# Optimization experiments

Measured on AMD Instinct MI355X. Metric: run time of the kernel, lower is better.

Reference implementation:

```python
import jax, jax.numpy as jnp
import numpy as np

N_NODES = 100000
N_EDGES = 1200000
IN_FEATS = 30
HIDDEN = 64


def setup_inputs() -> dict:
    key = jax.random.key(0)
    k = jax.random.split(key, 6)
    x = jax.random.normal(k[0], (N_NODES, IN_FEATS), dtype=jnp.float32)
    W1 = jax.random.normal(k[1], (IN_FEATS, HIDDEN), dtype=jnp.float32) * (1.0 / np.sqrt(IN_FEATS))
    b1 = jnp.zeros((HIDDEN,), dtype=jnp.float32)
    W2 = jax.random.normal(k[2], (HIDDEN, HIDDEN), dtype=jnp.float32) * (1.0 / np.sqrt(HIDDEN))
    b2 = jnp.zeros((HIDDEN,), dtype=jnp.float32)
    src = jax.random.randint(k[3], (N_EDGES,), 0, N_NODES, dtype=jnp.int32)
    dst = jax.random.randint(k[4], (N_EDGES,), 0, N_NODES, dtype=jnp.int32)
    return {"x": x, "W1": W1, "b1": b1, "W2": W2, "b2": b2, "src": src, "dst": dst}


def _graph_conv(h, W, b, src, dst, norm_src, norm_dst, n_nodes):
    # DGL GraphConv, norm='both': D_in^{-1/2} A D_out^{-1/2} h W + b, then relu
    h = h * norm_src[:, None]          # [N, din] scale by out-degree^{-1/2}
    h = h @ W                          # [N, dout] dense transform
    agg = jax.ops.segment_sum(h[src], dst, num_segments=n_nodes)  # sparse aggregation
    return jax.nn.relu(agg * norm_dst[:, None] + b)


def reference(x, W1, b1, W2, b2, src, dst):
    n = x.shape[0]
    ones = jnp.ones(src.shape, dtype=x.dtype)
    out_deg = jax.ops.segment_sum(ones, src, num_segments=n)
    in_deg = jax.ops.segment_sum(ones, dst, num_segments=n)
    norm_src = jnp.maximum(out_deg, 1.0) ** -0.5
    norm_dst = jnp.maximum(in_deg, 1.0) ** -0.5
    h = _graph_conv(x, W1, b1, src, dst, norm_src, norm_dst, n)
    h = _graph_conv(h, W2, b2, src, dst, norm_src, norm_dst, n)
    return h
```

## Files before the change

kernel.cpp:

```cpp
#include <hip/hip_runtime.h>
#include <hip/hip_fp16.h>

constexpr int IN_FEATS = 30;
constexpr int HIDDEN   = 64;
constexpr int SCAN_CHUNK = 1024;
constexpr int RB_BITS = 9;
constexpr int RB_MASK = (1 << RB_BITS) - 1;
constexpr int ECHUNK  = 2048;
constexpr int NPB     = 32;

__global__ __launch_bounds__(256) void part_count(
    const int* __restrict__ src, const int* __restrict__ dst,
    int* __restrict__ cntT, int nE, int NBK, int NCH, int NK2)
{
    __shared__ int binsD[256], binsS[256];
    int b = blockIdx.x, t = threadIdx.x;
    binsD[t] = 0; binsS[t] = 0;
    __syncthreads();
    int base = b * ECHUNK;
#pragma unroll
    for (int i = 0; i < ECHUNK / 256; ++i) {
        int e = base + t + i * 256;
        if (e < nE) {
            atomicAdd(&binsD[dst[e] >> RB_BITS], 1);
            atomicAdd(&binsS[src[e] >> RB_BITS], 1);
        }
    }
    __syncthreads();
    if (t < NBK) {
        cntT[t * NCH + b]       = binsD[t];
        cntT[NK2 + t * NCH + b] = binsS[t];
    }
}

__global__ __launch_bounds__(256) void scan_partial(
    const int* __restrict__ deg, int* __restrict__ blockSum, int n)
{
    __shared__ int part[256];
    int b = blockIdx.x, t = threadIdx.x;
    int base = b * SCAN_CHUNK + t * 4;
    int s = 0;
#pragma unroll
    for (int j = 0; j < 4; ++j) { int i = base + j; if (i < n) s += deg[i]; }
    part[t] = s;
    __syncthreads();
    for (int off = 1; off < 256; off <<= 1) {
        int add = (t >= off) ? part[t - off] : 0;
        __syncthreads();
        part[t] += add;
        __syncthreads();
    }
    if (t == 255) blockSum[b] = part[255];
}

__global__ __launch_bounds__(1024) void scan_offsets(int* blockSum, int nB, int* totalPtr)
{
    __shared__ int part[1024];
    int t = threadIdx.x;
    int v = (t < nB) ? blockSum[t] : 0;
    part[t] = v;
    __syncthreads();
    for (int off = 1; off < 1024; off <<= 1) {
        int add = (t >= off) ? part[t - off] : 0;
        __syncthreads();
        part[t] += add;
        __syncthreads();
    }
    if (t < nB) blockSum[t] = part[t] - v;
    if (totalPtr && t == nB - 1) *totalPtr = part[t];
}

__global__ __launch_bounds__(256) void scan_final(
    const int* __restrict__ deg, const int* __restrict__ blockSum,
    int* __restrict__ outp, int n)
{
    __shared__ int part[256];
    int b = blockIdx.x, t = threadIdx.x;
    int base = b * SCAN_CHUNK + t * 4;
    int v[4];
    int s = 0;
#pragma unroll
    for (int j = 0; j < 4; ++j) { int i = base + j; v[j] = (i < n) ? deg[i] : 0; s += v[j]; }
    part[t] = s;
    __syncthreads();
    for (int off = 1; off < 256; off <<= 1) {
        int add = (t >= off) ? part[t - off] : 0;
        __syncthreads();
        part[t] += add;
        __syncthreads();
    }
    int run = blockSum[b] + part[t] - s;
#pragma unroll
    for (int j = 0; j < 4; ++j) {
        int i = base + j;
        if (i < n) outp[i] = run;
        run += v[j];
    }
}

__global__ __launch_bounds__(256) void part_scatter(
    const int* __restrict__ src, const int* __restrict__ dst,
    const int* __restrict__ ofsT, unsigned int* __restrict__ pairs,
    int nE, int NBK, int NCH)
{
    __shared__ int bins[256], lstart[256], lcur[256], gofs[256], part[256];
    __shared__ int lsrc[ECHUNK], ldst[ECHUNK];
    int b = blockIdx.x, t = threadIdx.x;
    bins[t] = 0;
    if (t < NBK) gofs[t] = ofsT[t * NCH + b];
    __syncthreads();
    int base = b * ECHUNK;
    int rs[ECHUNK / 256], rd[ECHUNK / 256];
#pragma unroll
    for (int i = 0; i < ECHUNK / 256; ++i) {
        int e = base + t + i * 256;
        rs[i] = -1;
        if (e < nE) {
            rs[i] = src[e]; rd[i] = dst[e];
            atomicAdd(&bins[rd[i] >> RB_BITS], 1);
        }
    }
    __syncthreads();
    int v = bins[t];
    part[t] = v;
    __syncthreads();
    for (int off = 1; off < 256; off <<= 1) {
        int add = (t >= off) ? part[t - off] : 0;
        __syncthreads();
        part[t] += add;
        __syncthreads();
    }
    lstart[t] = part[t] - v;
    lcur[t]   = part[t] - v;
    __syncthreads();
#pragma unroll
    for (int i = 0; i < ECHUNK / 256; ++i) {
        if (rs[i] >= 0) {
            int k = rd[i] >> RB_BITS;
            int p = atomicAdd(&lcur[k], 1);
            lsrc[p] = rs[i]; ldst[p] = rd[i];
        }
    }
    __syncthreads();
    int cE = min(ECHUNK, nE - base);
    for (int j = t; j < cE; j += 256) {
        int d = ldst[j], k = d >> RB_BITS;
        int g = gofs[k] + (j - lstart[k]);
        pairs[g] = ((unsigned int)(d & RB_MASK) << 23) | (unsigned int)lsrc[j];
    }
}

__global__ __launch_bounds__(256) void srcpart_scatter(
    const int* __restrict__ src, const int* __restrict__ ofsT,
    unsigned short* __restrict__ sloc, int nE, int NBK, int NCH, int NK2)
{
    __shared__ int cur[256];
    int b = blockIdx.x, t = threadIdx.x;
    if (t < NBK) cur[t] = ofsT[NK2 + t * NCH + b] - nE;
    __syncthreads();
    int base = b * ECHUNK;
#pragma unroll
    for (int i = 0; i < ECHUNK / 256; ++i) {
        int e = base + t + i * 256;
        if (e < nE) {
            int s = src[e];
            int pos = atomicAdd(&cur[s >> RB_BITS], 1);
            sloc[pos] = (unsigned short)(s & RB_MASK);
        }
    }
}

__global__ __launch_bounds__(256) void bucket_histD(
    const unsigned int* __restrict__ pairs, const int* __restrict__ ofsT,
    int* __restrict__ degI, int nE, int n, int NBK, int NCH)
{
    __shared__ int bins[512];
    int k = blockIdx.x, t = threadIdx.x;
    bins[t] = 0; bins[t + 256] = 0;
    __syncthreads();
    int begin = ofsT[k * NCH];
    int end   = (k + 1 < NBK) ? ofsT[(k + 1) * NCH] : nE;
    for (int e = begin + t; e < end; e += 256)
        atomicAdd(&bins[pairs[e] >> 23], 1);
    __syncthreads();
    int base = k << RB_BITS;
    if (base + t < n)       degI[base + t]       = bins[t];
    if (base + 256 + t < n) degI[base + 256 + t] = bins[t + 256];
}

__global__ __launch_bounds__(256) void bucket_histS(
    const unsigned short* __restrict__ sloc, const int* __restrict__ ofsT,
    int* __restrict__ degO, int nE, int n, int NBK, int NCH, int NK2)
{
    __shared__ int bins[512];
    int k = blockIdx.x, t = threadIdx.x;
    bins[t] = 0; bins[t + 256] = 0;
    __syncthreads();
    int begin = ofsT[NK2 + k * NCH] - nE;
    int end   = (k + 1 < NBK) ? (ofsT[NK2 + (k + 1) * NCH] - nE) : nE;
    for (int e = begin + t; e < end; e += 256)
        atomicAdd(&bins[sloc[e]], 1);
    __syncthreads();
    int base = k << RB_BITS;
    if (base + t < n)       degO[base + t]       = bins[t];
    if (base + 256 + t < n) degO[base + 256 + t] = bins[t + 256];
}

__global__ __launch_bounds__(256) void csr_place(
    const unsigned int* __restrict__ pairs, const int* __restrict__ ofsT,
    const int* __restrict__ rowptr, int* __restrict__ csr,
    int nE, int n, int NBK, int NCH)
{
    __shared__ int cur[512];
    int k = blockIdx.x, t = threadIdx.x;
    int base = k << RB_BITS;
    int node = base + t;
    cur[t] = (node < n) ? rowptr[node] : 0;
    node += 256;
    cur[t + 256] = (node < n) ? rowptr[node] : 0;
    __syncthreads();
    int begin = ofsT[k * NCH];
    int end   = (k + 1 < NBK) ? ofsT[(k + 1) * NCH] : nE;
    for (int e = begin + t; e < end; e += 256) {
        unsigned int u = pairs[e];
        int p = atomicAdd(&cur[u >> 23], 1);
        csr[p] = (int)(u & 0x7FFFFFu);
    }
}

__global__ __launch_bounds__(256) void xn_prep(
    const float* __restrict__ x, const int* __restrict__ degO,
    unsigned int* __restrict__ xn, int n)
{
    int tid = blockIdx.x * 256 + threadIdx.x;
    int node = tid >> 4, p = tid & 15;
    if (node >= n) return;
    float ns = rsqrtf(fmaxf((float)degO[node], 1.0f));
    float a = (2 * p     < IN_FEATS) ? x[(size_t)node * IN_FEATS + 2 * p]     * ns : 0.0f;
    float b = (2 * p + 1 < IN_FEATS) ? x[(size_t)node * IN_FEATS + 2 * p + 1] * ns : 0.0f;
    __half2 h = __floats2half2_rn(a, b);
    xn[(size_t)node * 16 + p] = *reinterpret_cast<unsigned int*>(&h);
}

__global__ __launch_bounds__(256) void gather_x2(
    const unsigned int* __restrict__ xn, const int* __restrict__ csr,
    const int* __restrict__ rowptr, float* __restrict__ aggx, int n)
{
    int wv   = (blockIdx.x * 256 + threadIdx.x) >> 6;
    int lane = threadIdx.x & 63;
    if (wv >= n) return;
    int begin = rowptr[wv], end = rowptr[wv + 1];
    int g = lane >> 3;
    int p = lane & 7;
    float a0 = 0, a1 = 0, a2 = 0, a3 = 0;
    int e = begin + g;
    for (; e + 8 < end; e += 16) {
        int s0 = csr[e], s1 = csr[e + 8];
        uint2 u0 = *reinterpret_cast<const uint2*>(xn + (size_t)s0 * 16 + 2 * p);
        uint2 u1 = *reinterpret_cast<const uint2*>(xn + (size_t)s1 * 16 + 2 * p);
        float2 v;
        v = __half22float2(*reinterpret_cast<__half2*>(&u0.x)); a0 += v.x; a1 += v.y;
        v = __half22float2(*reinterpret_cast<__half2*>(&u0.y)); a2 += v.x; a3 += v.y;
        v = __half22float2(*reinterpret_cast<__half2*>(&u1.x)); a0 += v.x; a1 += v.y;
        v = __half22float2(*reinterpret_cast<__half2*>(&u1.y)); a2 += v.x; a3 += v.y;
    }
    if (e < end) {
        int s0 = csr[e];
        uint2 u0 = *reinterpret_cast<const uint2*>(xn + (size_t)s0 * 16 + 2 * p);
        float2 v;
        v = __half22float2(*reinterpret_cast<__half2*>(&u0.x)); a0 += v.x; a1 += v.y;
        v = __half22float2(*reinterpret_cast<__half2*>(&u0.y)); a2 += v.x; a3 += v.y;
    }
    a0 += __shfl_xor(a0, 8);  a1 += __shfl_xor(a1, 8);  a2 += __shfl_xor(a2, 8);  a3 += __shfl_xor(a3, 8);
    a0 += __shfl_xor(a0, 16); a1 += __shfl_xor(a1, 16); a2 += __shfl_xor(a2, 16); a3 += __shfl_xor(a3, 16);
    a0 += __shfl_xor(a0, 32); a1 += __shfl_xor(a1, 32); a2 += __shfl_xor(a2, 32); a3 += __shfl_xor(a3, 32);
    if (g == 0) {
        float4 r = make_float4(a0, a1, a2, a3);
        *reinterpret_cast<float4*>(aggx + (size_t)wv * 32 + 4 * p) = r;
    }
}

__global__ __launch_bounds__(256) void transform1(
    const float* __restrict__ aggx, const float* __restrict__ W1,
    const float* __restrict__ b1, const int* __restrict__ degI,
    const int* __restrict__ degO, unsigned int* __restrict__ h1s, int n)
{
    __shared__ float w[32 * HIDDEN];
    __shared__ float rows[NPB][32];
    int t = threadIdx.x;
    int node0 = blockIdx.x * NPB;
    {
        const float4* w4 = (const float4*)W1;
        float4* lw4 = (float4*)w;
#pragma unroll
        for (int i = 0; i < 2; ++i) {
            int idx = t + 256 * i;
            if (idx < 480)      lw4[idx] = w4[idx];
            else if (idx < 512) lw4[idx] = make_float4(0.f, 0.f, 0.f, 0.f);
        }
    }
    {
        int node = node0 + (t >> 3);
        if (node < n)
            *reinterpret_cast<float4*>(&rows[t >> 3][(t & 7) * 4]) =
                *reinterpret_cast<const float4*>(aggx + (size_t)node * 32 + (t & 7) * 4);
    }
    __syncthreads();
    int f = t & 63, g = t >> 6;
    float acc[8] = {0, 0, 0, 0, 0, 0, 0, 0};
#pragma unroll 2
    for (int k = 0; k < 32; k += 4) {
        float w0 = w[(k + 0) * 64 + f], w1 = w[(k + 1) * 64 + f];
        float w2v = w[(k + 2) * 64 + f], w3 = w[(k + 3) * 64 + f];
#pragma unroll
        for (int j = 0; j < 8; ++j) {
            float4 rv = *reinterpret_cast<const float4*>(&rows[g * 8 + j][k]);
            acc[j] = fmaf(rv.x, w0, acc[j]);
            acc[j] = fmaf(rv.y, w1, acc[j]);
            acc[j] = fmaf(rv.z, w2v, acc[j]);
            acc[j] = fmaf(rv.w, w3, acc[j]);
        }
    }
    float bv = b1[f];
#pragma unroll
    for (int j = 0; j < 8; ++j) {
        int node = node0 + g * 8 + j;
        float hv = 0.0f;
        if (node < n) {
            float ndv = rsqrtf(fmaxf((float)degI[node], 1.0f));
            float nsv = rsqrtf(fmaxf((float)degO[node], 1.0f));
            hv = fmaxf(fmaf(acc[j], ndv, bv), 0.0f) * nsv;
        }
        float hv1 = __shfl_down(hv, 1);
        if (node < n && (f & 1) == 0) {
            __half2 h = __floats2half2_rn(hv, hv1);
            h1s[(size_t)node * 32 + (f >> 1)] = *reinterpret_cast<unsigned int*>(&h);
        }
    }
}

__global__ __launch_bounds__(256) void gather_h2(
    const unsigned int* __restrict__ h, const int* __restrict__ csr,
    const int* __restrict__ rowptr, float* __restrict__ agg, int n)
{
    int wv   = (blockIdx.x * 256 + threadIdx.x) >> 6;
    int lane = threadIdx.x & 63;
    if (wv >= n) return;
    int begin = rowptr[wv], end = rowptr[wv + 1];
    int g = lane >> 4;
    int p = lane & 15;
    float a0 = 0, a1 = 0, a2 = 0, a3 = 0;
    int e = begin + g;
    for (; e + 4 < end; e += 8) {
        int s0 = csr[e], s1 = csr[e + 4];
        uint2 u0 = *reinterpret_cast<const uint2*>(h + (size_t)s0 * 32 + 2 * p);
        uint2 u1 = *reinterpret_cast<const uint2*>(h + (size_t)s1 * 32 + 2 * p);
        float2 v;
        v = __half22float2(*reinterpret_cast<__half2*>(&u0.x)); a0 += v.x; a1 += v.y;
        v = __half22float2(*reinterpret_cast<__half2*>(&u0.y)); a2 += v.x; a3 += v.y;
        v = __half22float2(*reinterpret_cast<__half2*>(&u1.x)); a0 += v.x; a1 += v.y;
        v = __half22float2(*reinterpret_cast<__half2*>(&u1.y)); a2 += v.x; a3 += v.y;
    }
    if (e < end) {
        int s0 = csr[e];
        uint2 u0 = *reinterpret_cast<const uint2*>(h + (size_t)s0 * 32 + 2 * p);
        float2 v;
        v = __half22float2(*reinterpret_cast<__half2*>(&u0.x)); a0 += v.x; a1 += v.y;
        v = __half22float2(*reinterpret_cast<__half2*>(&u0.y)); a2 += v.x; a3 += v.y;
    }
    a0 += __shfl_xor(a0, 16); a1 += __shfl_xor(a1, 16); a2 += __shfl_xor(a2, 16); a3 += __shfl_xor(a3, 16);
    a0 += __shfl_xor(a0, 32); a1 += __shfl_xor(a1, 32); a2 += __shfl_xor(a2, 32); a3 += __shfl_xor(a3, 32);
    if (g == 0) {
        float4 r = make_float4(a0, a1, a2, a3);
        *reinterpret_cast<float4*>(agg + (size_t)wv * 64 + 4 * p) = r;
    }
}

__global__ __launch_bounds__(256) void transform2(
    float* aggout, const float* __restrict__ W2,
    const float* __restrict__ b2, const int* __restrict__ degI, int n)
{
    __shared__ float w[HIDDEN * HIDDEN];
    __shared__ float rows[NPB][HIDDEN];
    int t = threadIdx.x;
    int node0 = blockIdx.x * NPB;
    {
        const float4* w4 = (const float4*)W2;
        float4* lw4 = (float4*)w;
#pragma unroll
        for (int i = 0; i < 4; ++i) lw4[t + 256 * i] = w4[t + 256 * i];
    }
    {
#pragma unroll
        for (int i = 0; i < 2; ++i) {
            int idx = t + 256 * i;
            int node = node0 + (idx >> 4);
            if (node < n)
                *reinterpret_cast<float4*>(&rows[idx >> 4][(idx & 15) * 4]) =
                    *reinterpret_cast<const float4*>(aggout + (size_t)node * 64 + (idx & 15) * 4);
        }
    }
    __syncthreads();
    int f = t & 63, g = t >> 6;
    float acc[8] = {0, 0, 0, 0, 0, 0, 0, 0};
#pragma unroll 2
    for (int k = 0; k < 64; k += 4) {
        float w0 = w[(k + 0) * 64 + f], w1 = w[(k + 1) * 64 + f];
        float w2v = w[(k + 2) * 64 + f], w3 = w[(k + 3) * 64 + f];
#pragma unroll
        for (int j = 0; j < 8; ++j) {
            float4 rv = *reinterpret_cast<const float4*>(&rows[g * 8 + j][k]);
            acc[j] = fmaf(rv.x, w0, acc[j]);
            acc[j] = fmaf(rv.y, w1, acc[j]);
            acc[j] = fmaf(rv.z, w2v, acc[j]);
            acc[j] = fmaf(rv.w, w3, acc[j]);
        }
    }
    float bv = b2[f];
#pragma unroll
    for (int j = 0; j < 8; ++j) {
        int node = node0 + g * 8 + j;
        if (node < n) {
            float ndv = rsqrtf(fmaxf((float)degI[node], 1.0f));
            aggout[(size_t)node * 64 + f] = fmaxf(fmaf(acc[j], ndv, bv), 0.0f);
        }
    }
}

extern "C" void kernel_launch(void* const* d_in, const int* in_sizes, int n_in,
                              void* d_out, int out_size, void* d_ws, size_t ws_size,
                              hipStream_t stream)
{
    const float* x  = (const float*)d_in[0];
    const float* W1 = (const float*)d_in[1];
    const float* b1 = (const float*)d_in[2];
    const float* W2 = (const float*)d_in[3];
    const float* b2 = (const float*)d_in[4];
    const int*  src = (const int*)d_in[5];
    const int*  dst = (const int*)d_in[6];
    float* out = (float*)d_out;

    const int n  = in_sizes[0] / IN_FEATS;
    const int nE = in_sizes[5];

    const int NBK = (n + (1 << RB_BITS) - 1) >> RB_BITS;
    const int NCH = (nE + ECHUNK - 1) / ECHUNK;
    const int NK2 = NBK * NCH;

    const size_t poolWords = (size_t)n * 32;
    unsigned int* pairs = (unsigned int*)d_ws;
    int* cntT = (int*)d_ws + nE;
    int* bsum = cntT + 2 * NK2;
    unsigned short* sloc = (unsigned short*)(bsum + 1024);
    unsigned int* xn  = (unsigned int*)d_ws;
    unsigned int* h1s = (unsigned int*)d_ws;
    int* degO   = (int*)d_ws + poolWords;
    int* degI   = degO + n;
    int* rowptr = degI + n;
    int* csr    = rowptr + (n + 1);

    const int nB  = (n + SCAN_CHUNK - 1) / SCAN_CHUNK;
    const int nB2 = (2 * NK2 + SCAN_CHUNK - 1) / SCAN_CHUNK;
    const int waveBlocks = (n * 64 + 255) / 256;
    const int tfBlocks   = (n + NPB - 1) / NPB;

    part_count<<<NCH, 256, 0, stream>>>(src, dst, cntT, nE, NBK, NCH, NK2);
    scan_partial<<<nB2, 256, 0, stream>>>(cntT, bsum, 2 * NK2);
    scan_offsets<<<1, 1024, 0, stream>>>(bsum, nB2, nullptr);
    scan_final<<<nB2, 256, 0, stream>>>(cntT, bsum, cntT, 2 * NK2);

    part_scatter<<<NCH, 256, 0, stream>>>(src, dst, cntT, pairs, nE, NBK, NCH);
    srcpart_scatter<<<NCH, 256, 0, stream>>>(src, cntT, sloc, nE, NBK, NCH, NK2);

    bucket_histD<<<NBK, 256, 0, stream>>>(pairs, cntT, degI, nE, n, NBK, NCH);
    bucket_histS<<<NBK, 256, 0, stream>>>(sloc, cntT, degO, nE, n, NBK, NCH, NK2);

    scan_partial<<<nB, 256, 0, stream>>>(degI, bsum, n);
    scan_offsets<<<1, 1024, 0, stream>>>(bsum, nB, rowptr + n);
    scan_final<<<nB, 256, 0, stream>>>(degI, bsum, rowptr, n);
    csr_place<<<NBK, 256, 0, stream>>>(pairs, cntT, rowptr, csr, nE, n, NBK, NCH);

    xn_prep<<<(n * 16 + 255) / 256, 256, 0, stream>>>(x, degO, xn, n);
    gather_x2<<<waveBlocks, 256, 0, stream>>>(xn, csr, rowptr, out , n);
    transform1<<<tfBlocks, 256, 0, stream>>>(out, W1, b1, degI, degO, h1s, n);

    gather_h2<<<waveBlocks, 256, 0, stream>>>(h1s, csr, rowptr, out, n);
    transform2<<<tfBlocks, 256, 0, stream>>>(out, W2, b2, degI, n);
}
```

Measured before the change: 196.5 us.

## Fuse CSR build stages into fewer kernels, computing rowptr from bucket offsets

Folds the source-side scatter into part_scatter. Merges the destination histogram, the rowptr scan and CSR placement into one per-bucket kernel, using the bucket's global start offset plus a local prefix scan, so the global three-kernel scan goes away. Also fuses the out-degree histogram with the x normalisation and half-precision packing, and gives xn and h1s their own workspace regions instead of aliasing the pairs buffer. This removes six kernel launches and several global round trips, in exchange for a larger workspace footprint and more work per block in the bucket kernels.

```diff
diff --git a/kernel.cpp b/kernel.cpp
--- a/kernel.cpp
+++ b/kernel.cpp
@@ -101,13 +101,16 @@
 __global__ __launch_bounds__(256) void part_scatter(
     const int* __restrict__ src, const int* __restrict__ dst,
     const int* __restrict__ ofsT, unsigned int* __restrict__ pairs,
-    int nE, int NBK, int NCH)
-{
-    __shared__ int bins[256], lstart[256], lcur[256], gofs[256], part[256];
+    unsigned short* __restrict__ sloc, int nE, int NBK, int NCH, int NK2)
+{
+    __shared__ int bins[256], lstart[256], lcur[256], gofs[256], part[256], scur[256];
     __shared__ int lsrc[ECHUNK], ldst[ECHUNK];
     int b = blockIdx.x, t = threadIdx.x;
     bins[t] = 0;
-    if (t < NBK) gofs[t] = ofsT[t * NCH + b];
+    if (t < NBK) {
+        gofs[t] = ofsT[t * NCH + b];
+        scur[t] = ofsT[NK2 + t * NCH + b] - nE;
+    }
     __syncthreads();
     int base = b * ECHUNK;
     int rs[ECHUNK / 256], rd[ECHUNK / 256];
@@ -120,6 +123,14 @@
             atomicAdd(&bins[rd[i] >> RB_BITS], 1);
         }
     }
+#pragma unroll
+    for (int i = 0; i < ECHUNK / 256; ++i) {
+        if (rs[i] >= 0) {
+            int s = rs[i];
+            int pos = atomicAdd(&scur[s >> RB_BITS], 1);
+            sloc[pos] = (unsigned short)(s & RB_MASK);
+        }
+    }
     __syncthreads();
     int v = bins[t];
     part[t] = v;
@@ -150,31 +161,14 @@
     }
 }
 
-__global__ __launch_bounds__(256) void srcpart_scatter(
-    const int* __restrict__ src, const int* __restrict__ ofsT,
-    unsigned short* __restrict__ sloc, int nE, int NBK, int NCH, int NK2)
-{
-    __shared__ int cur[256];
-    int b = blockIdx.x, t = threadIdx.x;
-    if (t < NBK) cur[t] = ofsT[NK2 + t * NCH + b] - nE;
-    __syncthreads();
-    int base = b * ECHUNK;
-#pragma unroll
-    for (int i = 0; i < ECHUNK / 256; ++i) {
-        int e = base + t + i * 256;
-        if (e < nE) {
-            int s = src[e];
-            int pos = atomicAdd(&cur[s >> RB_BITS], 1);
-            sloc[pos] = (unsigned short)(s & RB_MASK);
-        }
-    }
-}
-
-__global__ __launch_bounds__(256) void bucket_histD(
+__global__ __launch_bounds__(256) void bucket_build(
     const unsigned int* __restrict__ pairs, const int* __restrict__ ofsT,
-    int* __restrict__ degI, int nE, int n, int NBK, int NCH)
+    int* __restrict__ degI, int* __restrict__ rowptr, int* __restrict__ csr,
+    int nE, int n, int NBK, int NCH)
 {
     __shared__ int bins[512];
+    __shared__ int part[256];
+    __shared__ int cur[512];
     int k = blockIdx.x, t = threadIdx.x;
     bins[t] = 0; bins[t + 256] = 0;
     __syncthreads();
@@ -183,14 +177,36 @@
     for (int e = begin + t; e < end; e += 256)
         atomicAdd(&bins[pairs[e] >> 23], 1);
     __syncthreads();
+    int v0 = bins[2 * t], v1 = bins[2 * t + 1];
+    int s = v0 + v1;
+    part[t] = s;
+    __syncthreads();
+    for (int off = 1; off < 256; off <<= 1) {
+        int add = (t >= off) ? part[t - off] : 0;
+        __syncthreads();
+        part[t] += add;
+        __syncthreads();
+    }
+    int pre = part[t] - s;
     int base = k << RB_BITS;
-    if (base + t < n)       degI[base + t]       = bins[t];
-    if (base + 256 + t < n) degI[base + 256 + t] = bins[t + 256];
-}
-
-__global__ __launch_bounds__(256) void bucket_histS(
+    int n0 = base + 2 * t, n1 = n0 + 1;
+    int r0 = begin + pre, r1 = r0 + v0;
+    cur[2 * t] = r0; cur[2 * t + 1] = r1;
+    if (n0 < n) { degI[n0] = v0; rowptr[n0] = r0; }
+    if (n1 < n) { degI[n1] = v1; rowptr[n1] = r1; }
+    if (k == NBK - 1 && t == 0) rowptr[n] = nE;
+    __syncthreads();
+    for (int e = begin + t; e < end; e += 256) {
+        unsigned int u = pairs[e];
+        int p = atomicAdd(&cur[u >> 23], 1);
+        csr[p] = (int)(u & 0x7FFFFFu);
+    }
+}
+
+__global__ __launch_bounds__(256) void bucket_srcside(
     const unsigned short* __restrict__ sloc, const int* __restrict__ ofsT,
-    int* __restrict__ degO, int nE, int n, int NBK, int NCH, int NK2)
+    const float* __restrict__ x, int* __restrict__ degO,
+    unsigned int* __restrict__ xn, int nE, int n, int NBK, int NCH, int NK2)
 {
     __shared__ int bins[512];
     int k = blockIdx.x, t = threadIdx.x;
@@ -204,42 +220,19 @@
     int base = k << RB_BITS;
     if (base + t < n)       degO[base + t]       = bins[t];
     if (base + 256 + t < n) degO[base + 256 + t] = bins[t + 256];
-}
-
-__global__ __launch_bounds__(256) void csr_place(
-    const unsigned int* __restrict__ pairs, const int* __restrict__ ofsT,
-    const int* __restrict__ rowptr, int* __restrict__ csr,
-    int nE, int n, int NBK, int NCH)
-{
-    __shared__ int cur[512];
-    int k = blockIdx.x, t = threadIdx.x;
-    int base = k << RB_BITS;
-    int node = base + t;
-    cur[t] = (node < n) ? rowptr[node] : 0;
-    node += 256;
-    cur[t + 256] = (node < n) ? rowptr[node] : 0;
-    __syncthreads();
-    int begin = ofsT[k * NCH];
-    int end   = (k + 1 < NBK) ? ofsT[(k + 1) * NCH] : nE;
-    for (int e = begin + t; e < end; e += 256) {
-        unsigned int u = pairs[e];
-        int p = atomicAdd(&cur[u >> 23], 1);
-        csr[p] = (int)(u & 0x7FFFFFu);
-    }
-}
-
-__global__ __launch_bounds__(256) void xn_prep(
-    const float* __restrict__ x, const int* __restrict__ degO,
-    unsigned int* __restrict__ xn, int n)
-{
-    int tid = blockIdx.x * 256 + threadIdx.x;
-    int node = tid >> 4, p = tid & 15;
-    if (node >= n) return;
-    float ns = rsqrtf(fmaxf((float)degO[node], 1.0f));
-    float a = (2 * p     < IN_FEATS) ? x[(size_t)node * IN_FEATS + 2 * p]     * ns : 0.0f;
-    float b = (2 * p + 1 < IN_FEATS) ? x[(size_t)node * IN_FEATS + 2 * p + 1] * ns : 0.0f;
-    __half2 h = __floats2half2_rn(a, b);
-    xn[(size_t)node * 16 + p] = *reinterpret_cast<unsigned int*>(&h);
+#pragma unroll 4
+    for (int i = 0; i < 32; ++i) {
+        int idx = t + 256 * i;
+        int nl = idx >> 4, p = idx & 15;
+        int node = base + nl;
+        if (node < n) {
+            float ns = rsqrtf(fmaxf((float)bins[nl], 1.0f));
+            float a = (2 * p     < IN_FEATS) ? x[(size_t)node * IN_FEATS + 2 * p]     * ns : 0.0f;
+            float b = (2 * p + 1 < IN_FEATS) ? x[(size_t)node * IN_FEATS + 2 * p + 1] * ns : 0.0f;
+            __half2 h = __floats2half2_rn(a, b);
+            xn[(size_t)node * 16 + p] = *reinterpret_cast<unsigned int*>(&h);
+        }
+    }
 }
 
 __global__ __launch_bounds__(256) void gather_x2(
@@ -447,19 +440,17 @@
     const int NCH = (nE + ECHUNK - 1) / ECHUNK;
     const int NK2 = NBK * NCH;
 
-    const size_t poolWords = (size_t)n * 32;
     unsigned int* pairs = (unsigned int*)d_ws;
     int* cntT = (int*)d_ws + nE;
     int* bsum = cntT + 2 * NK2;
     unsigned short* sloc = (unsigned short*)(bsum + 1024);
-    unsigned int* xn  = (unsigned int*)d_ws;
-    unsigned int* h1s = (unsigned int*)d_ws;
-    int* degO   = (int*)d_ws + poolWords;
+    unsigned int* xn  = (unsigned int*)(bsum + 1024) + (nE + 1) / 2;
+    unsigned int* h1s = xn + (size_t)n * 16;
+    int* degO   = (int*)(h1s + (size_t)n * 32);
     int* degI   = degO + n;
     int* rowptr = degI + n;
     int* csr    = rowptr + (n + 1);
 
-    const int nB  = (n + SCAN_CHUNK - 1) / SCAN_CHUNK;
     const int nB2 = (2 * NK2 + SCAN_CHUNK - 1) / SCAN_CHUNK;
     const int waveBlocks = (n * 64 + 255) / 256;
     const int tfBlocks   = (n + NPB - 1) / NPB;
@@ -469,18 +460,11 @@
     scan_offsets<<<1, 1024, 0, stream>>>(bsum, nB2, nullptr);
     scan_final<<<nB2, 256, 0, stream>>>(cntT, bsum, cntT, 2 * NK2);
 
-    part_scatter<<<NCH, 256, 0, stream>>>(src, dst, cntT, pairs, nE, NBK, NCH);
-    srcpart_scatter<<<NCH, 256, 0, stream>>>(src, cntT, sloc, nE, NBK, NCH, NK2);
-
-    bucket_histD<<<NBK, 256, 0, stream>>>(pairs, cntT, degI, nE, n, NBK, NCH);
-    bucket_histS<<<NBK, 256, 0, stream>>>(sloc, cntT, degO, nE, n, NBK, NCH, NK2);
-
-    scan_partial<<<nB, 256, 0, stream>>>(degI, bsum, n);
-    scan_offsets<<<1, 1024, 0, stream>>>(bsum, nB, rowptr + n);
-    scan_final<<<nB, 256, 0, stream>>>(degI, bsum, rowptr, n);
-    csr_place<<<NBK, 256, 0, stream>>>(pairs, cntT, rowptr, csr, nE, n, NBK, NCH);
-
-    xn_prep<<<(n * 16 + 255) / 256, 256, 0, stream>>>(x, degO, xn, n);
+    part_scatter<<<NCH, 256, 0, stream>>>(src, dst, cntT, pairs, sloc, nE, NBK, NCH, NK2);
+
+    bucket_build<<<NBK, 256, 0, stream>>>(pairs, cntT, degI, rowptr, csr, nE, n, NBK, NCH);
+    bucket_srcside<<<NBK, 256, 0, stream>>>(sloc, cntT, x, degO, xn, nE, n, NBK, NCH, NK2);
+
     gather_x2<<<waveBlocks, 256, 0, stream>>>(xn, csr, rowptr, out , n);
     transform1<<<tfBlocks, 256, 0, stream>>>(out, W1, b1, degI, degO, h1s, n);
 
```

Result: faster. 192.1 us (-2.2%).
